# Kernel tuning notes

Measured on AMD Instinct MI355X. Metric: run time of the kernel, lower is better.

The kernel has to match this reference:

```python
import jax, jax.numpy as jnp
import numpy as np

B, SEQ, DIM, HEADS = 2, 2048, 512, 8
HD = DIM // HEADS
RANK, DFF = 128, 1024
TAU_MEM, TAU_ADAPT, SLOPE, EPS = 0.99, 0.95, 25.0, 1e-6
THRESH, ADAPT_STRENGTH = 0.5, 0.1
TREE_LEVELS = int(np.log2(SEQ))  # 11


def rmsnorm(x, w, eps=EPS):
    return x * jax.lax.rsqrt(jnp.mean(x * x, axis=-1, keepdims=True) + eps) * w


def rope_cos_sin(seq, hd):
    inv = 1.0 / (10000.0 ** (jnp.arange(0, hd, 2, dtype=jnp.float32) / hd))
    f = jnp.arange(seq, dtype=jnp.float32)[:, None] * inv[None, :]  # [S, hd/2]
    emb = jnp.concatenate([f, f], axis=-1)  # [S, hd]
    return jnp.cos(emb), jnp.sin(emb)


def apply_rope(x, cos, sin):
    # x: [B, H, S, hd]; rotate-half formulation
    x1, x2 = jnp.split(x, 2, axis=-1)
    return x * cos + jnp.concatenate([-x2, x1], axis=-1) * sin


def setup_inputs() -> dict:
    key = jax.random.key(0)
    ks = jax.random.split(key, 12)
    w = lambda k, shape, fan: (jax.random.normal(k, shape, jnp.float32) / np.sqrt(fan))
    return {
        "x": jax.random.normal(ks[0], (B, SEQ, DIM), jnp.float32),
        "norm_w": jnp.ones((DIM,), jnp.float32),
        "wq": w(ks[1], (DIM, DIM), DIM),
        "wk": w(ks[2], (DIM, DIM), DIM),
        "wv": w(ks[3], (DIM, DIM), DIM),
        "wo": w(ks[4], (DIM, DIM), DIM),
        "lat_w": w(ks[5], (SEQ, SEQ), SEQ),
        "bt": jnp.full((DIM,), THRESH, jnp.float32),
        "as_w": jnp.full((DIM,), ADAPT_STRENGTH, jnp.float32),
        "gate_w": w(ks[6], (DIM, DIM), DIM),
        "tnorm1_w": jnp.ones((DIM,), jnp.float32),
        "tnorm2_w": jnp.ones((DIM,), jnp.float32),
        "ffn_norm_w": jnp.ones((DIM,), jnp.float32),
        "u_w": w(ks[7], (DIM, RANK), DIM),
        "v_w": w(ks[8], (RANK, 2 * DFF), RANK),
        "down_w": w(ks[9], (DFF, DIM), DFF),
    }


def reference(x, norm_w, wq, wk, wv, wo, lat_w, bt, as_w, gate_w,
              tnorm1_w, tnorm2_w, ffn_norm_w, u_w, v_w, down_w):
    Bx, S, D = x.shape
    # --- pre-norm + QKV projections (base_proj) ---
    h = rmsnorm(x, norm_w)
    q = (h @ wq.T).reshape(Bx, S, HEADS, HD).transpose(0, 2, 1, 3)  # [B,H,S,hd]
    k = (h @ wk.T).reshape(Bx, S, HEADS, HD).transpose(0, 2, 1, 3)
    v = (h @ wv.T).reshape(Bx, S, HEADS, HD).transpose(0, 2, 1, 3)
    # --- RoPE ---
    cos, sin = rope_cos_sin(S, HD)
    q = apply_rope(q, cos, sin)
    k = apply_rope(k, cos, sin)
    # --- causal self-attention ---
    scores = jnp.einsum("bhqd,bhkd->bhqk", q, k) / np.sqrt(HD)
    causal = jnp.tril(jnp.ones((S, S), bool))
    scores = jnp.where(causal, scores, jnp.float32(-1e9))
    attn = jnp.einsum("bhqk,bhkd->bhqd", jax.nn.softmax(scores, axis=-1), v)
    attn = attn.transpose(0, 2, 1, 3).reshape(Bx, S, D) @ wo.T
    # --- causal lateral mixing across sequence ---
    mixed = jnp.einsum("ts,bsd->btd", jnp.tril(lat_w), attn)
    # --- ALIF spiking recurrence over the sequence (soft surrogate spike) ---
    def alif_step(carry, i_t):
        vmem, ad = carry
        vmem = TAU_MEM * vmem + i_t
        th = bt + as_w * ad
        spike = jax.nn.sigmoid(SLOPE * (vmem - th))
        vmem = vmem - spike * th          # soft reset
        ad = TAU_ADAPT * ad + spike        # threshold adaptation
        return (vmem, ad), spike
    init = (jnp.zeros((Bx, D), x.dtype), jnp.zeros((Bx, D), x.dtype))
    _, spikes = jax.lax.scan(alif_step, init, mixed.transpose(1, 0, 2))
    spikes = spikes.transpose(1, 0, 2)  # [B,S,D]
    # --- fused addadd residual ---
    h2 = x + mixed + spikes
    # --- binary-tree cell recursion to a root summary ---
    s = h2
    for _ in range(TREE_LEVELS):
        raw = s[:, 0::2, :] + s[:, 1::2, :]         # pairwise sums (raw_sums)
        res = 0.5 * raw                              # residual / prev_s surrogate
        n = rmsnorm(raw, tnorm1_w)
        g = jax.nn.sigmoid(n @ gate_w.T)
        s = rmsnorm(g * n + (1.0 - g) * res, tnorm2_w)
    h3 = h2 + s[:, 0:1, :]  # broadcast root back over the sequence
    # --- low-rank SwiGLU FFN ---
    hn = rmsnorm(h3, ffn_norm_w)
    up = (hn @ u_w) @ v_w                 # [B,S,2*DFF]
    a, b = jnp.split(up, 2, axis=-1)
    ffn = (jax.nn.silu(a) * b) @ down_w   # [B,S,D]
    return h3 + ffn
```

## Files before the change

kernel.cpp:

```cpp
#include <hip/hip_runtime.h>
#include <math.h>

#define BB 2
#define SS 2048
#define DD 512
#define HH 8
#define HDD 64
#define RANKK 128
#define DFFF 1024

typedef short bf16x8 __attribute__((ext_vector_type(8)));
typedef float f32x4 __attribute__((ext_vector_type(4)));

__device__ __forceinline__ short f2b(float f) {
  union { float f; unsigned u; } v; v.f = f;
  unsigned r = v.u + 0x7FFF + ((v.u >> 16) & 1);
  return (short)(r >> 16);
}
__device__ __forceinline__ float b2f(short s) {
  union { unsigned u; float f; } v; v.u = ((unsigned)(unsigned short)s) << 16;
  return v.f;
}

__device__ __forceinline__ void gll16(const void* g, void* l) {
  __builtin_amdgcn_global_load_lds(
      (const __attribute__((address_space(1))) unsigned int*)g,
      (__attribute__((address_space(3))) unsigned int*)l, 16, 0, 0);
}
__device__ __forceinline__ void gll4(const void* g, void* l) {
  __builtin_amdgcn_global_load_lds(
      (const __attribute__((address_space(1))) unsigned int*)g,
      (__attribute__((address_space(3))) unsigned int*)l, 4, 0, 0);
}

__device__ __forceinline__ float wsum(float v) {
#pragma unroll
  for (int off = 32; off > 0; off >>= 1) v += __shfl_xor(v, off, 64);
  return v;
}

__global__ void splitw(const float* __restrict__ in, short* __restrict__ hi,
                       short* __restrict__ lo, int n) {
  int i = (blockIdx.x * 256 + threadIdx.x) * 4;
  if (i >= n) return;
  float4 v = *(const float4*)(in + i);
  short4 h4, l4;
  h4.x = f2b(v.x); l4.x = f2b(v.x - b2f(h4.x));
  h4.y = f2b(v.y); l4.y = f2b(v.y - b2f(h4.y));
  h4.z = f2b(v.z); l4.z = f2b(v.z - b2f(h4.z));
  h4.w = f2b(v.w); l4.w = f2b(v.w - b2f(h4.w));
  *(short4*)(hi + i) = h4;
  *(short4*)(lo + i) = l4;
}

__global__ void cvtb(const float* __restrict__ in, short* __restrict__ out, int n) {
  int i = (blockIdx.x * 256 + threadIdx.x) * 4;
  if (i >= n) return;
  float4 v = *(const float4*)(in + i);
  short4 o; o.x = f2b(v.x); o.y = f2b(v.y); o.z = f2b(v.z); o.w = f2b(v.w);
  *(short4*)(out + i) = o;
}

__global__ void sum2(const float* __restrict__ a, const float* __restrict__ bq,
                     float* __restrict__ o) {
  int i = (blockIdx.x * 256 + threadIdx.x) * 4;
  float4 va = *(const float4*)(a + i);
  float4 vb = *(const float4*)(bq + i);
  float4 vo = {va.x + vb.x, va.y + vb.y, va.z + vb.z, va.w + vb.w};
  *(float4*)(o + i) = vo;
}

__global__ void transp_cvt(const float* __restrict__ in, short* __restrict__ out,
                           int R, int C) {
  __shared__ float t[32][33];
  int c0 = blockIdx.x * 32, r0 = blockIdx.y * 32;
#pragma unroll
  for (int i = 0; i < 4; i++) {
    int idx = threadIdx.x + i * 256;
    int r = idx >> 5, c = idx & 31;
    t[r][c] = in[(size_t)(r0 + r) * C + c0 + c];
  }
  __syncthreads();
#pragma unroll
  for (int i = 0; i < 4; i++) {
    int idx = threadIdx.x + i * 256;
    int cc = idx >> 5, rr = idx & 31;
    out[(size_t)(c0 + cc) * R + r0 + rr] = f2b(t[rr][cc]);
  }
}

__global__ void rmsnorm_hl(const float* __restrict__ x, const float* __restrict__ w,
                           short* __restrict__ oh, short* __restrict__ ol, int rows) {
  int wid = blockIdx.x * 4 + (threadIdx.x >> 6);
  int lane = threadIdx.x & 63;
  if (wid >= rows) return;
  const float* xp = x + (size_t)wid * DD + lane * 8;
  float4 a = *(const float4*)xp;
  float4 b = *(const float4*)(xp + 4);
  float ss = a.x*a.x + a.y*a.y + a.z*a.z + a.w*a.w
           + b.x*b.x + b.y*b.y + b.z*b.z + b.w*b.w;
  ss = wsum(ss);
  float r = rsqrtf(ss * (1.0f / DD) + 1e-6f);
  const float* wp = w + lane * 8;
  float4 wa = *(const float4*)wp, wb = *(const float4*)(wp + 4);
  float o8[8] = {a.x*r*wa.x, a.y*r*wa.y, a.z*r*wa.z, a.w*r*wa.w,
                 b.x*r*wb.x, b.y*r*wb.y, b.z*r*wb.z, b.w*r*wb.w};
  short hv[8], lv[8];
#pragma unroll
  for (int i = 0; i < 8; i++) { hv[i] = f2b(o8[i]); lv[i] = f2b(o8[i] - b2f(hv[i])); }
  short* op = oh + (size_t)wid * DD + lane * 8;
  short* lp = ol + (size_t)wid * DD + lane * 8;
  *(short4*)op = make_short4(hv[0], hv[1], hv[2], hv[3]);
  *(short4*)(op + 4) = make_short4(hv[4], hv[5], hv[6], hv[7]);
  *(short4*)lp = make_short4(lv[0], lv[1], lv[2], lv[3]);
  *(short4*)(lp + 4) = make_short4(lv[4], lv[5], lv[6], lv[7]);
}

template <bool SPL, int OM, bool ROPE>
__global__ __launch_bounds__(256) void ggemm(const short* __restrict__ Ah_g,
                                             const short* __restrict__ Al_g,
                                             const short* __restrict__ Bh_g,
                                             const short* __restrict__ Bl_g,
                                             const float* __restrict__ ADD,
                                             void* __restrict__ C, void* __restrict__ C2,
                                             int M, int N, int K) {
  __shared__ short Ahs[128 * 32];
  __shared__ short Bhs[128 * 32];
  __shared__ short Als[SPL ? 128 * 32 : 8];
  __shared__ short Bls[SPL ? 128 * 32 : 8];
  const int tid = threadIdx.x, l = tid & 63, w = tid >> 6;
  const int wr = (w >> 1) * 64, wc = (w & 1) * 64;
  const int bm = blockIdx.y * 128, bn = blockIdx.x * 128;
  f32x4 acc[4][4] = {};
  for (int k0 = 0; k0 < K; k0 += 32) {
#pragma unroll
    for (int p = 0; p < 2; p++) {
      int row = p * 64 + (tid >> 2), g = tid & 3;
      int swz = (g ^ ((row >> 1) & 3)) * 8;
      gll16(Ah_g + (size_t)(bm + row) * K + k0 + swz, Ahs + p * 2048 + tid * 8);
      gll16(Bh_g + (size_t)(bn + row) * K + k0 + swz, Bhs + p * 2048 + tid * 8);
      if (SPL) {
        gll16(Al_g + (size_t)(bm + row) * K + k0 + swz, Als + p * 2048 + tid * 8);
        gll16(Bl_g + (size_t)(bn + row) * K + k0 + swz, Bls + p * 2048 + tid * 8);
      }
    }
    __syncthreads();
    bf16x8 ah[4], bh[4], al[4], bl[4];
#pragma unroll
    for (int m = 0; m < 4; m++) {
      int r = wr + m * 16 + (l & 15);
      int go = (((l >> 4) ^ ((r >> 1) & 3)) << 3);
      ah[m] = *(const bf16x8*)(Ahs + r * 32 + go);
      if (SPL) al[m] = *(const bf16x8*)(Als + r * 32 + go);
    }
#pragma unroll
    for (int n = 0; n < 4; n++) {
      int r = wc + n * 16 + (l & 15);
      int go = (((l >> 4) ^ ((r >> 1) & 3)) << 3);
      bh[n] = *(const bf16x8*)(Bhs + r * 32 + go);
      if (SPL) bl[n] = *(const bf16x8*)(Bls + r * 32 + go);
    }
#pragma unroll
    for (int m = 0; m < 4; m++)
#pragma unroll
      for (int n = 0; n < 4; n++) {
        acc[m][n] = __builtin_amdgcn_mfma_f32_16x16x32_bf16(ah[m], bh[n], acc[m][n], 0, 0, 0);
        if (SPL) {
          acc[m][n] = __builtin_amdgcn_mfma_f32_16x16x32_bf16(ah[m], bl[n], acc[m][n], 0, 0, 0);
          acc[m][n] = __builtin_amdgcn_mfma_f32_16x16x32_bf16(al[m], bh[n], acc[m][n], 0, 0, 0);
        }
      }
    __syncthreads();
  }
  const int ll = l & 15, lg4 = (l >> 4) * 4;
  if (ROPE) {
#pragma unroll
    for (int m = 0; m < 4; m++)
#pragma unroll
      for (int n = 0; n < 2; n++) {
        int i_ = n * 16 + ll;
        float inv = exp2f(-(float)i_ * (13.287712379549449f / 32.0f));
#pragma unroll
        for (int j = 0; j < 4; j++) {
          int gm = bm + wr + m * 16 + lg4 + j;
          int s = gm & (SS - 1);
          float ang = (float)s * inv;
          float sn, cs;
          sincosf(ang, &sn, &cs);
          float v1 = acc[m][n][j], v2 = acc[m][n + 2][j];
          acc[m][n][j]     = v1 * cs - v2 * sn;
          acc[m][n + 2][j] = v2 * cs + v1 * sn;
        }
      }
  }
#pragma unroll
  for (int m = 0; m < 4; m++)
#pragma unroll
    for (int n = 0; n < 4; n++) {
      int gn = bn + wc + n * 16 + ll;
#pragma unroll
      for (int j = 0; j < 4; j++) {
        int gm = bm + wr + m * 16 + lg4 + j;
        if (gm >= M || gn >= N) continue;
        float v = acc[m][n][j];
        if (OM == 0) {
          ((float*)C)[(size_t)gm * N + gn] = v;
        } else if (OM == 1) {
          ((short*)C)[(size_t)gm * N + gn] = f2b(v);
        } else if (OM == 6) {
          size_t off = (size_t)gm * N + gn;
          ((float*)C)[off] = v + ADD[off];
        } else {
          short hi = f2b(v);
          short lo = f2b(v - b2f(hi));
          int b = gm >> 11, s = gm & (SS - 1);
          int hh2 = gn >> 6, d = gn & 63;
          size_t off;
          if (OM == 2)      off = (((size_t)(b * HH + hh2)) * SS + s) * 64 + d;
          else if (OM == 3) off = (((size_t)(b * HH + hh2)) * 64 + d) * SS + s;
          else              off = ((size_t)(b * DD) + gn) * SS + s;
          ((short*)C)[off] = hi;
          ((short*)C2)[off] = lo;
        }
      }
    }
}

__global__ __launch_bounds__(256) void qkv_g(const short* __restrict__ Ah_g,
                                             const short* __restrict__ Al_g,
                                             const short* __restrict__ wh0, const short* __restrict__ wl0,
                                             const short* __restrict__ wh1, const short* __restrict__ wl1,
                                             const short* __restrict__ wh2, const short* __restrict__ wl2,
                                             short* __restrict__ c0h, short* __restrict__ c0l,
                                             short* __restrict__ c1h, short* __restrict__ c1l,
                                             short* __restrict__ c2h, short* __restrict__ c2l) {
  const int z = blockIdx.z;
  const short* Bh_g = (z == 0) ? wh0 : (z == 1) ? wh1 : wh2;
  const short* Bl_g = (z == 0) ? wl0 : (z == 1) ? wl1 : wl2;
  short* Ch = (z == 0) ? c0h : (z == 1) ? c1h : c2h;
  short* Cl = (z == 0) ? c0l : (z == 1) ? c1l : c2l;
  const int K = DD;
  __shared__ short Ahs[128 * 32];
  __shared__ short Bhs[128 * 32];
  __shared__ short Als[128 * 32];
  __shared__ short Bls[128 * 32];
  const int tid = threadIdx.x, l = tid & 63, w = tid >> 6;
  const int wr = (w >> 1) * 64, wc = (w & 1) * 64;
  const int bm = blockIdx.y * 128, bn = blockIdx.x * 128;
  f32x4 acc[4][4] = {};
  for (int k0 = 0; k0 < K; k0 += 32) {
#pragma unroll
    for (int p = 0; p < 2; p++) {
      int row = p * 64 + (tid >> 2), g = tid & 3;
      int swz = (g ^ ((row >> 1) & 3)) * 8;
      gll16(Ah_g + (size_t)(bm + row) * K + k0 + swz, Ahs + p * 2048 + tid * 8);
      gll16(Bh_g + (size_t)(bn + row) * K + k0 + swz, Bhs + p * 2048 + tid * 8);
      gll16(Al_g + (size_t)(bm + row) * K + k0 + swz, Als + p * 2048 + tid * 8);
      gll16(Bl_g + (size_t)(bn + row) * K + k0 + swz, Bls + p * 2048 + tid * 8);
    }
    __syncthreads();
    bf16x8 ah[4], bh[4], al[4], bl[4];
#pragma unroll
    for (int m = 0; m < 4; m++) {
      int r = wr + m * 16 + (l & 15);
      int go = (((l >> 4) ^ ((r >> 1) & 3)) << 3);
      ah[m] = *(const bf16x8*)(Ahs + r * 32 + go);
      al[m] = *(const bf16x8*)(Als + r * 32 + go);
    }
#pragma unroll
    for (int n = 0; n < 4; n++) {
      int r = wc + n * 16 + (l & 15);
      int go = (((l >> 4) ^ ((r >> 1) & 3)) << 3);
      bh[n] = *(const bf16x8*)(Bhs + r * 32 + go);
      bl[n] = *(const bf16x8*)(Bls + r * 32 + go);
    }
#pragma unroll
    for (int m = 0; m < 4; m++)
#pragma unroll
      for (int n = 0; n < 4; n++) {
        acc[m][n] = __builtin_amdgcn_mfma_f32_16x16x32_bf16(ah[m], bh[n], acc[m][n], 0, 0, 0);
        acc[m][n] = __builtin_amdgcn_mfma_f32_16x16x32_bf16(ah[m], bl[n], acc[m][n], 0, 0, 0);
        acc[m][n] = __builtin_amdgcn_mfma_f32_16x16x32_bf16(al[m], bh[n], acc[m][n], 0, 0, 0);
      }
    __syncthreads();
  }
  const int ll = l & 15, lg4 = (l >> 4) * 4;
  if (z < 2) {
#pragma unroll
    for (int m = 0; m < 4; m++)
#pragma unroll
      for (int n = 0; n < 2; n++) {
        int i_ = n * 16 + ll;
        float inv = exp2f(-(float)i_ * (13.287712379549449f / 32.0f));
#pragma unroll
        for (int j = 0; j < 4; j++) {
          int gm = bm + wr + m * 16 + lg4 + j;
          int s = gm & (SS - 1);
          float ang = (float)s * inv;
          float sn, cs;
          sincosf(ang, &sn, &cs);
          float v1 = acc[m][n][j], v2 = acc[m][n + 2][j];
          acc[m][n][j]     = v1 * cs - v2 * sn;
          acc[m][n + 2][j] = v2 * cs + v1 * sn;
        }
      }
  }
#pragma unroll
  for (int m = 0; m < 4; m++)
#pragma unroll
    for (int n = 0; n < 4; n++) {
      int gn = bn + wc + n * 16 + ll;
#pragma unroll
      for (int j = 0; j < 4; j++) {
        int gm = bm + wr + m * 16 + lg4 + j;
        float v = acc[m][n][j];
        short hi = f2b(v);
        short lo = f2b(v - b2f(hi));
        int b = gm >> 11, s = gm & (SS - 1);
        int hh2 = gn >> 6, d = gn & 63;
        size_t off = (z < 2) ? ((((size_t)(b * HH + hh2)) * SS + s) * 64 + d)
                             : ((((size_t)(b * HH + hh2)) * 64 + d) * SS + s);
        Ch[off] = hi;
        Cl[off] = lo;
      }
    }
}

__global__ __launch_bounds__(256) void lat_g(const float* __restrict__ lat,
                                             const short* __restrict__ bTh,
                                             const short* __restrict__ bTl,
                                             float* __restrict__ P0,
                                             float* __restrict__ P1) {
  const int zb = blockIdx.z >> 1;
  const int half = blockIdx.z & 1;
  bTh += (size_t)zb * DD * SS;
  bTl += (size_t)zb * DD * SS;
  float* Cc = (half == 0 ? P0 : P1) + (size_t)zb * DD * SS;
  __shared__ short Ah[128 * 32];
  __shared__ short Al[128 * 32];
  __shared__ short Bh[128 * 32];
  __shared__ short Bl[128 * 32];
  const int tid = threadIdx.x, l = tid & 63, w = tid >> 6;
  const int wr = (w >> 1) * 64, wc = (w & 1) * 64;
  const int bm = blockIdx.y * 128, bn = blockIdx.x * 128;
  const int T = blockIdx.y + 1;
  const int h0 = (T + 1) >> 1;
  const int kbeg = (half == 0) ? 0 : h0 * 128;
  const int kend = (half == 0) ? h0 * 128 : T * 128;
  f32x4 acc[4][4] = {};
  const int ll = l & 15, lg4 = (l >> 4) * 4;
  for (int k0 = kbeg; k0 < kend; k0 += 32) {
#pragma unroll
    for (int p = 0; p < 2; p++) {
      int row = p * 64 + (tid >> 2), g = tid & 3;
      int swz = (g ^ ((row >> 1) & 3)) * 8;
      gll16(bTh + (size_t)(bn + row) * SS + k0 + swz, Bh + p * 2048 + tid * 8);
      gll16(bTl + (size_t)(bn + row) * SS + k0 + swz, Bl + p * 2048 + tid * 8);
    }
#pragma unroll
    for (int i = 0; i < 4; i++) {
      int lin = i * 256 + tid;
      int row = lin >> 3, f4 = lin & 7;
      int gr = bm + row;
      float4 v = *(const float4*)(lat + (size_t)gr * SS + k0 + f4 * 4);
      int kc = k0 + f4 * 4;
      if (kc + 0 > gr) v.x = 0.0f;
      if (kc + 1 > gr) v.y = 0.0f;
      if (kc + 2 > gr) v.z = 0.0f;
      if (kc + 3 > gr) v.w = 0.0f;
      int off = row * 32 + (((f4 >> 1) ^ ((row >> 1) & 3)) << 3) + (f4 & 1) * 4;
      short4 hh, lo;
      hh.x = f2b(v.x); lo.x = f2b(v.x - b2f(hh.x));
      hh.y = f2b(v.y); lo.y = f2b(v.y - b2f(hh.y));
      hh.z = f2b(v.z); lo.z = f2b(v.z - b2f(hh.z));
      hh.w = f2b(v.w); lo.w = f2b(v.w - b2f(hh.w));
      *(short4*)(Ah + off) = hh;
      *(short4*)(Al + off) = lo;
    }
    __syncthreads();
    bf16x8 ah[4], bh[4], al[4], bl[4];
#pragma unroll
    for (int m = 0; m < 4; m++) {
      int r = wr + m * 16 + (l & 15);
      int go = (((l >> 4) ^ ((r >> 1) & 3)) << 3);
      ah[m] = *(const bf16x8*)(Ah + r * 32 + go);
      al[m] = *(const bf16x8*)(Al + r * 32 + go);
    }
#pragma unroll
    for (int n = 0; n < 4; n++) {
      int r = wc + n * 16 + (l & 15);
      int go = (((l >> 4) ^ ((r >> 1) & 3)) << 3);
      bh[n] = *(const bf16x8*)(Bh + r * 32 + go);
      bl[n] = *(const bf16x8*)(Bl + r * 32 + go);
    }
#pragma unroll
    for (int m = 0; m < 4; m++)
#pragma unroll
      for (int n = 0; n < 4; n++) {
        acc[m][n] = __builtin_amdgcn_mfma_f32_16x16x32_bf16(ah[m], bh[n], acc[m][n], 0, 0, 0);
        acc[m][n] = __builtin_amdgcn_mfma_f32_16x16x32_bf16(ah[m], bl[n], acc[m][n], 0, 0, 0);
        acc[m][n] = __builtin_amdgcn_mfma_f32_16x16x32_bf16(al[m], bh[n], acc[m][n], 0, 0, 0);
      }
    __syncthreads();
  }
#pragma unroll
  for (int m = 0; m < 4; m++)
#pragma unroll
    for (int n = 0; n < 4; n++) {
      int gn = bn + wc + n * 16 + ll;
#pragma unroll
      for (int j = 0; j < 4; j++) {
        int gm = bm + wr + m * 16 + lg4 + j;
        Cc[(size_t)gn * SS + gm] = acc[m][n][j];
      }
    }
}

__global__ __launch_bounds__(256) void attn_g(const short* __restrict__ qh,
                                              const short* __restrict__ ql,
                                              const short* __restrict__ kh,
                                              const short* __restrict__ kl,
                                              const short* __restrict__ vh,
                                              const short* __restrict__ vl,
                                              short* __restrict__ aho,
                                              short* __restrict__ alo) {
  const int h = blockIdx.y, b = blockIdx.z;
  const int qt = (b == 0) ? (int)blockIdx.x : 31 - (int)blockIdx.x;
  const int q0 = qt * 64;
  const int tid = threadIdx.x, w = tid >> 6, l = tid & 63;
  const int lg = l >> 4, ll = l & 15;
  __shared__ short Kh[64 * 64], Kl[64 * 64];
  __shared__ short Vh[64 * 64], Vl[64 * 64];
  __shared__ short Ph[64 * 64], Pl[64 * 64];
  const size_t bh = (size_t)(b * HH + h);

  const int qr = q0 + w * 16 + ll;
  const short* qbh = qh + (bh * SS + qr) * 64;
  const short* qbl = ql + (bh * SS + qr) * 64;
  bf16x8 qfh[2], qfl[2];
#pragma unroll
  for (int ks = 0; ks < 2; ks++) {
    qfh[ks] = *(const bf16x8*)(qbh + (ks * 4 + lg) * 8);
    qfl[ks] = *(const bf16x8*)(qbl + (ks * 4 + lg) * 8);
  }

  f32x4 o[4] = {};
  float mrow[4] = {-1e30f, -1e30f, -1e30f, -1e30f};
  float lsum[4] = {};
  const int qrow0 = q0 + w * 16 + lg * 4;
  const int ntiles = qt + 1;

  for (int kt = 0; kt < ntiles; kt++) {
#pragma unroll
    for (int p = 0; p < 2; p++) {
      int row = p * 32 + (tid >> 3), g = tid & 7;
      int sw = ((g ^ (row & 7)) << 3);
      size_t krow = (bh * SS + kt * 64 + row) * 64;
      size_t vrow = (bh * 64 + row) * SS + kt * 64;
      gll16(kh + krow + sw, Kh + p * 2048 + tid * 8);
      gll16(kl + krow + sw, Kl + p * 2048 + tid * 8);
      gll16(vh + vrow + sw, Vh + p * 2048 + tid * 8);
      gll16(vl + vrow + sw, Vl + p * 2048 + tid * 8);
    }
    __syncthreads();

    f32x4 sv[4] = {};
#pragma unroll
    for (int nf = 0; nf < 4; nf++) {
      int r = nf * 16 + ll;
#pragma unroll
      for (int ks = 0; ks < 2; ks++) {
        int g = (ks * 4 + lg) ^ (r & 7);
        bf16x8 khf = *(const bf16x8*)(Kh + r * 64 + g * 8);
        bf16x8 klf = *(const bf16x8*)(Kl + r * 64 + g * 8);
        sv[nf] = __builtin_amdgcn_mfma_f32_16x16x32_bf16(qfh[ks], khf, sv[nf], 0, 0, 0);
        sv[nf] = __builtin_amdgcn_mfma_f32_16x16x32_bf16(qfh[ks], klf, sv[nf], 0, 0, 0);
        sv[nf] = __builtin_amdgcn_mfma_f32_16x16x32_bf16(qfl[ks], khf, sv[nf], 0, 0, 0);
      }
    }
#pragma unroll
    for (int nf = 0; nf < 4; nf++) {
      int kpos = kt * 64 + nf * 16 + ll;
#pragma unroll
      for (int j = 0; j < 4; j++) {
        float v = sv[nf][j] * 0.125f;
        sv[nf][j] = (kpos > qrow0 + j) ? -1e30f : v;
      }
    }
    float cf[4];
#pragma unroll
    for (int j = 0; j < 4; j++) {
      float r = fmaxf(fmaxf(sv[0][j], sv[1][j]), fmaxf(sv[2][j], sv[3][j]));
      r = fmaxf(r, __shfl_xor(r, 1)); r = fmaxf(r, __shfl_xor(r, 2));
      r = fmaxf(r, __shfl_xor(r, 4)); r = fmaxf(r, __shfl_xor(r, 8));
      float mn = fmaxf(mrow[j], r);
      cf[j] = __expf(mrow[j] - mn);
      mrow[j] = mn;
    }
    float ps[4] = {};
#pragma unroll
    for (int nf = 0; nf < 4; nf++)
#pragma unroll
      for (int j = 0; j < 4; j++) {
        float p = __expf(sv[nf][j] - mrow[j]);
        sv[nf][j] = p;
        ps[j] += p;
      }
#pragma unroll
    for (int j = 0; j < 4; j++) {
      float r = ps[j];
      r += __shfl_xor(r, 1); r += __shfl_xor(r, 2);
      r += __shfl_xor(r, 4); r += __shfl_xor(r, 8);
      lsum[j] = lsum[j] * cf[j] + r;
    }
#pragma unroll
    for (int nf = 0; nf < 4; nf++)
#pragma unroll
      for (int j = 0; j < 4; j++) o[nf][j] *= cf[j];
#pragma unroll
    for (int nf = 0; nf < 4; nf++)
#pragma unroll
      for (int j = 0; j < 4; j++) {
        int rowP = w * 16 + lg * 4 + j;
        int col = nf * 16 + ll;
        int off = rowP * 64 + (((col >> 3) ^ (rowP & 7)) << 3) + (col & 7);
        float p = sv[nf][j];
        short hi = f2b(p);
        Ph[off] = hi;
        Pl[off] = f2b(p - b2f(hi));
      }
    __syncthreads();
    bf16x8 pfh[2], pfl[2];
    {
      int rowA = w * 16 + ll;
#pragma unroll
      for (int ks = 0; ks < 2; ks++) {
        int g = (ks * 4 + lg) ^ (rowA & 7);
        pfh[ks] = *(const bf16x8*)(Ph + rowA * 64 + g * 8);
        pfl[ks] = *(const bf16x8*)(Pl + rowA * 64 + g * 8);
      }
    }
#pragma unroll
    for (int nf = 0; nf < 4; nf++) {
      int r = nf * 16 + ll;
#pragma unroll
      for (int ks = 0; ks < 2; ks++) {
        int g = (ks * 4 + lg) ^ (r & 7);
        bf16x8 vhf = *(const bf16x8*)(Vh + r * 64 + g * 8);
        bf16x8 vlf = *(const bf16x8*)(Vl + r * 64 + g * 8);
        o[nf] = __builtin_amdgcn_mfma_f32_16x16x32_bf16(pfh[ks], vhf, o[nf], 0, 0, 0);
        o[nf] = __builtin_amdgcn_mfma_f32_16x16x32_bf16(pfh[ks], vlf, o[nf], 0, 0, 0);
        o[nf] = __builtin_amdgcn_mfma_f32_16x16x32_bf16(pfl[ks], vhf, o[nf], 0, 0, 0);
      }
    }
    __syncthreads();
  }
  float inv[4];
#pragma unroll
  for (int j = 0; j < 4; j++) inv[j] = 1.0f / lsum[j];
#pragma unroll
  for (int nf = 0; nf < 4; nf++)
#pragma unroll
    for (int j = 0; j < 4; j++) {
      float v = o[nf][j] * inv[j];
      short hi = f2b(v);
      size_t off = ((size_t)(b * SS + qrow0 + j)) * DD + h * HDD + nf * 16 + ll;
      aho[off] = hi;
      alo[off] = f2b(v - b2f(hi));
    }
}

#define ACH 32
__global__ __launch_bounds__(64, 1) void tsa_alif5(const float* __restrict__ mixedT,
                                                   const float* __restrict__ bt,
                                                   const float* __restrict__ asw,
                                                   float* __restrict__ spikesT) {
  __shared__ float lds[2][ACH * 64];
  const int t = threadIdx.x;
  const int tid = blockIdx.x * 64 + t;
  const int b = tid >> 9, d = tid & 511;
  const float btd = bt[d], asd = asw[d];
  const float C = 36.06737602222409f;
  const float bt36 = btd * C, as36 = asd * C;
  const float bt99 = 0.99f * btd, as99 = 0.99f * asd;
  const size_t base = ((size_t)(b * DD + d)) * SS;
  const float* mp = mixedT + base;
  float* sp = spikesT + base;
#pragma unroll
  for (int j = 0; j < ACH; j++) gll4(mp + j, &lds[0][j * 64]);
  float vR = 0.0f, ad = 0.0f;
  for (int c = 0; c < SS / ACH; c++) {
    const int cur = c & 1;
    __syncthreads();
    if (c + 1 < SS / ACH) {
      const float* q = mp + (c + 1) * ACH;
#pragma unroll
      for (int j = 0; j < ACH; j++) gll4(q + j, &lds[cur ^ 1][j * 64]);
    }
    float m[ACH];
#pragma unroll
    for (int j = 0; j < ACH; j++) m[j] = lds[cur][j * 64 + t];
    vR += m[0];
    float sO[ACH];
#pragma unroll
    for (int j = 0; j < ACH; j++) {
      float thC = fmaf(ad, as36, bt36);
      float th99 = fmaf(ad, as99, bt99);
      float arg = fmaf(vR, -C, thC);
      float e = exp2f(arg);
      float s = __builtin_amdgcn_rcpf(1.0f + e);
      sO[j] = s;
      float pre = (j + 1 < ACH) ? fmaf(0.99f, vR, m[j + 1]) : (0.99f * vR);
      vR = fmaf(-th99, s, pre);
      ad = fmaf(0.95f, ad, s);
      if ((j & 3) == 3) {
        float4 o4 = {sO[j - 3], sO[j - 2], sO[j - 1], sO[j]};
        *(float4*)(sp + c * ACH + (j - 3)) = o4;
      }
    }
  }
}

__global__ __launch_bounds__(256) void fuse_h2(const float* __restrict__ x,
                                               const float* __restrict__ mixedT,
                                               const float* __restrict__ spikesT,
                                               float* __restrict__ h2) {
  const int s0 = blockIdx.x * 64, d0 = blockIdx.y * 64, b = blockIdx.z;
  __shared__ float t[64][65];
#pragma unroll
  for (int k = 0; k < 4; k++) {
    int dl = threadIdx.x >> 2;
    int sl = (threadIdx.x & 3) * 16 + k * 4;
    size_t off = ((size_t)(b * DD + d0 + dl)) * SS + s0 + sl;
    float4 mv = *(const float4*)(mixedT + off);
    float4 sv = *(const float4*)(spikesT + off);
    t[dl][sl + 0] = mv.x + sv.x;
    t[dl][sl + 1] = mv.y + sv.y;
    t[dl][sl + 2] = mv.z + sv.z;
    t[dl][sl + 3] = mv.w + sv.w;
  }
  __syncthreads();
#pragma unroll
  for (int k = 0; k < 4; k++) {
    int sl = threadIdx.x >> 2;
    int dl = (threadIdx.x & 3) * 16 + k * 4;
    size_t off = ((size_t)(b * SS + s0 + sl)) * DD + d0 + dl;
    float4 xv = *(const float4*)(x + off);
    float4 o;
    o.x = xv.x + t[dl + 0][sl];
    o.y = xv.y + t[dl + 1][sl];
    o.z = xv.z + t[dl + 2][sl];
    o.w = xv.w + t[dl + 3][sl];
    *(float4*)(h2 + off) = o;
  }
}

__global__ void tree_reduce_b(const float* __restrict__ sin_, const float* __restrict__ tn1,
                              short* __restrict__ nb, int Sn) {
  int wid = blockIdx.x * 4 + (threadIdx.x >> 6);
  int lane = threadIdx.x & 63;
  int rows = BB * Sn;
  if (wid >= rows) return;
  int b = wid / Sn, j = wid - b * Sn;
  const float* r0 = sin_ + ((size_t)(b * 2 * Sn + 2 * j)) * DD + lane * 8;
  const float* r1 = r0 + DD;
  float4 a0 = *(const float4*)r0, a1 = *(const float4*)(r0 + 4);
  float4 b0 = *(const float4*)r1, b1 = *(const float4*)(r1 + 4);
  float ra[8] = {a0.x + b0.x, a0.y + b0.y, a0.z + b0.z, a0.w + b0.w,
                 a1.x + b1.x, a1.y + b1.y, a1.z + b1.z, a1.w + b1.w};
  float ss = 0.0f;
#pragma unroll
  for (int i = 0; i < 8; i++) ss += ra[i] * ra[i];
  ss = wsum(ss);
  float rms = rsqrtf(ss * (1.0f / DD) + 1e-6f);
  const float* wp = tn1 + lane * 8;
  float4 wa = *(const float4*)wp, wb = *(const float4*)(wp + 4);
  float wv8[8] = {wa.x, wa.y, wa.z, wa.w, wb.x, wb.y, wb.z, wb.w};
  short* np = nb + (size_t)wid * DD + lane * 8;
  short4 n0, n1;
  n0.x = f2b(ra[0]*rms*wv8[0]); n0.y = f2b(ra[1]*rms*wv8[1]);
  n0.z = f2b(ra[2]*rms*wv8[2]); n0.w = f2b(ra[3]*rms*wv8[3]);
  n1.x = f2b(ra[4]*rms*wv8[4]); n1.y = f2b(ra[5]*rms*wv8[5]);
  n1.z = f2b(ra[6]*rms*wv8[6]); n1.w = f2b(ra[7]*rms*wv8[7]);
  *(short4*)np = n0;
  *(short4*)(np + 4) = n1;
}

__global__ void tree_combine_b(const float* __restrict__ g, const short* __restrict__ nb,
                               const float* __restrict__ sin_, const float* __restrict__ tn2,
                               float* __restrict__ sout, int Sn) {
  int wid = blockIdx.x * 4 + (threadIdx.x >> 6);
  int lane = threadIdx.x & 63;
  int rows = BB * Sn;
  if (wid >= rows) return;
  int b = wid / Sn, j = wid - b * Sn;
  const float* r0 = sin_ + ((size_t)(b * 2 * Sn + 2 * j)) * DD + lane * 8;
  const float* r1 = r0 + DD;
  float4 a0 = *(const float4*)r0, a1 = *(const float4*)(r0 + 4);
  float4 b0 = *(const float4*)r1, b1 = *(const float4*)(r1 + 4);
  float res[8] = {0.5f*(a0.x + b0.x), 0.5f*(a0.y + b0.y), 0.5f*(a0.z + b0.z), 0.5f*(a0.w + b0.w),
                  0.5f*(a1.x + b1.x), 0.5f*(a1.y + b1.y), 0.5f*(a1.z + b1.z), 0.5f*(a1.w + b1.w)};
  size_t base = (size_t)wid * DD + lane * 8;
  float t[8];
  float ss = 0.0f;
#pragma unroll
  for (int i = 0; i < 8; i++) {
    float gg = 1.0f / (1.0f + expf(-g[base + i]));
    float tv = gg * b2f(nb[base + i]) + (1.0f - gg) * res[i];
    t[i] = tv;
    ss += tv * tv;
  }
  ss = wsum(ss);
  float rms = rsqrtf(ss * (1.0f / DD) + 1e-6f);
#pragma unroll
  for (int i = 0; i < 8; i++) sout[base + i] = t[i] * rms * tn2[lane * 8 + i];
}

__global__ void h3hn_b(const float* __restrict__ h2, const float* __restrict__ root,
                       const float* __restrict__ fw, float* __restrict__ h3,
                       short* __restrict__ hn) {
  int wid = blockIdx.x * 4 + (threadIdx.x >> 6);
  int lane = threadIdx.x & 63;
  int b = wid >> 11;
  size_t base = (size_t)wid * DD + lane * 8;
  const float* rp = root + (size_t)b * DD + lane * 8;
  float t[8];
  float ss = 0.0f;
#pragma unroll
  for (int i = 0; i < 8; i++) {
    float tv = h2[base + i] + rp[i];
    t[i] = tv;
    ss += tv * tv;
    h3[base + i] = tv;
  }
  ss = wsum(ss);
  float rms = rsqrtf(ss * (1.0f / DD) + 1e-6f);
#pragma unroll
  for (int i = 0; i < 8; i++) hn[base + i] = f2b(t[i] * rms * fw[lane * 8 + i]);
}

__global__ __launch_bounds__(256) void upgate_g(const short* __restrict__ A,
                                                const short* __restrict__ Bv,
                                                short* __restrict__ ffa) {
  __shared__ short Ahs[128 * 32];
  __shared__ short B1s[128 * 32];
  __shared__ short B2s[128 * 32];
  const int tid = threadIdx.x, l = tid & 63, w = tid >> 6;
  const int wr = (w >> 1) * 64, wc = (w & 1) * 64;
  const int bm = blockIdx.y * 128, bn = blockIdx.x * 128;
  f32x4 acc1[4][4] = {}, acc2[4][4] = {};
  for (int k0 = 0; k0 < RANKK; k0 += 32) {
#pragma unroll
    for (int p = 0; p < 2; p++) {
      int row = p * 64 + (tid >> 2), g = tid & 3;
      int swz = (g ^ ((row >> 1) & 3)) * 8;
      gll16(A + (size_t)(bm + row) * RANKK + k0 + swz, Ahs + p * 2048 + tid * 8);
      gll16(Bv + (size_t)(bn + row) * RANKK + k0 + swz, B1s + p * 2048 + tid * 8);
      gll16(Bv + (size_t)(DFFF + bn + row) * RANKK + k0 + swz, B2s + p * 2048 + tid * 8);
    }
    __syncthreads();
    bf16x8 ah[4], b1[4], b2[4];
#pragma unroll
    for (int m = 0; m < 4; m++) {
      int r = wr + m * 16 + (l & 15);
      int go = (((l >> 4) ^ ((r >> 1) & 3)) << 3);
      ah[m] = *(const bf16x8*)(Ahs + r * 32 + go);
    }
#pragma unroll
    for (int n = 0; n < 4; n++) {
      int r = wc + n * 16 + (l & 15);
      int go = (((l >> 4) ^ ((r >> 1) & 3)) << 3);
      b1[n] = *(const bf16x8*)(B1s + r * 32 + go);
      b2[n] = *(const bf16x8*)(B2s + r * 32 + go);
    }
#pragma unroll
    for (int m = 0; m < 4; m++)
#pragma unroll
      for (int n = 0; n < 4; n++) {
        acc1[m][n] = __builtin_amdgcn_mfma_f32_16x16x32_bf16(ah[m], b1[n], acc1[m][n], 0, 0, 0);
        acc2[m][n] = __builtin_amdgcn_mfma_f32_16x16x32_bf16(ah[m], b2[n], acc2[m][n], 0, 0, 0);
      }
    __syncthreads();
  }
#pragma unroll
  for (int m = 0; m < 4; m++)
#pragma unroll
    for (int n = 0; n < 4; n++) {
      int gn = bn + wc + n * 16 + (l & 15);
#pragma unroll
      for (int j = 0; j < 4; j++) {
        int gm = bm + wr + m * 16 + (l >> 4) * 4 + j;
        float a = acc1[m][n][j];
        float s = a / (1.0f + __expf(-a));
        ffa[(size_t)gm * DFFF + gn] = f2b(s * acc2[m][n][j]);
      }
    }
}

extern "C" void kernel_launch(void* const* d_in, const int* in_sizes, int n_in,
                              void* d_out, int out_size, void* d_ws, size_t ws_size,
                              hipStream_t stream) {
  const float* x   = (const float*)d_in[0];
  const float* nw  = (const float*)d_in[1];
  const float* wq  = (const float*)d_in[2];
  const float* wk  = (const float*)d_in[3];
  const float* wv  = (const float*)d_in[4];
  const float* wo  = (const float*)d_in[5];
  const float* lat = (const float*)d_in[6];
  const float* btp = (const float*)d_in[7];
  const float* asw = (const float*)d_in[8];
  const float* gw  = (const float*)d_in[9];
  const float* tn1 = (const float*)d_in[10];
  const float* tn2 = (const float*)d_in[11];
  const float* fnw = (const float*)d_in[12];
  const float* uw  = (const float*)d_in[13];
  const float* vw  = (const float*)d_in[14];
  const float* dw  = (const float*)d_in[15];
  float* out = (float*)d_out;
  char* W = (char*)d_ws;
  const size_t MB = 1u << 20;

  short* h_hi = (short*)(W);
  short* h_lo = (short*)(W + 4 * MB);
  short* attn_hi = h_hi;
  short* attn_lo = h_lo;
  short* nb = (short*)(W);
  float* gb = (float*)(W + 2 * MB);
  short* q_hi = (short*)(W + 8 * MB);
  short* q_lo = (short*)(W + 12 * MB);
  short* apT_hi = q_hi;
  short* apT_lo = q_lo;
  float* spikesT = (float*)(W + 8 * MB);
  float* s0 = (float*)(W + 8 * MB);
  float* s1 = (float*)(W + 12 * MB);
  short* k_hi = (short*)(W + 16 * MB);
  short* k_lo = (short*)(W + 20 * MB);
  float* latP1 = (float*)(W + 16 * MB);
  short* hn = (short*)(W + 16 * MB);
  short* t1 = (short*)(W + 20 * MB);
  short* v_hi = (short*)(W + 24 * MB);
  short* v_lo = (short*)(W + 28 * MB);
  float* h2 = (float*)(W + 24 * MB);
  short* ffa = (short*)(W + 24 * MB);
  float* latP0 = (float*)(W + 32 * MB);
  short* gwb = (short*)(W + 32 * MB);
  short* uwT = gwb + 262144;
  short* vwT = uwT + 65536;
  short* dwT = vwT + 262144;

  short* wqh = (short*)out;
  short* wql = wqh + 262144;
  short* wkh = wql + 262144;
  short* wkl = wkh + 262144;
  short* wvh = wkl + 262144;
  short* wvl = wvh + 262144;
  short* woh = wvl + 262144;
  short* wol = woh + 262144;

  const int rows = BB * SS;

  splitw<<<256, 256, 0, stream>>>(wq, wqh, wql, DD * DD);
  splitw<<<256, 256, 0, stream>>>(wk, wkh, wkl, DD * DD);
  splitw<<<256, 256, 0, stream>>>(wv, wvh, wvl, DD * DD);
  splitw<<<256, 256, 0, stream>>>(wo, woh, wol, DD * DD);

  rmsnorm_hl<<<rows / 4, 256, 0, stream>>>(x, nw, h_hi, h_lo, rows);

  qkv_g<<<dim3(4, 32, 3), 256, 0, stream>>>(h_hi, h_lo,
                                            wqh, wql, wkh, wkl, wvh, wvl,
                                            q_hi, q_lo, k_hi, k_lo, v_hi, v_lo);

  attn_g<<<dim3(32, HH, BB), 256, 0, stream>>>(q_hi, q_lo, k_hi, k_lo, v_hi, v_lo,
                                               attn_hi, attn_lo);

  ggemm<true, 4, false><<<dim3(4, 32), 256, 0, stream>>>(
      attn_hi, attn_lo, woh, wol, nullptr, apT_hi, apT_lo, rows, DD, DD);

  lat_g<<<dim3(4, 16, 4), 256, 0, stream>>>(lat, apT_hi, apT_lo, latP0, latP1);

  sum2<<<(BB * DD * SS / 4) / 256, 256, 0, stream>>>(latP0, latP1, latP0);

  tsa_alif5<<<16, 64, 0, stream>>>(latP0, btp, asw, spikesT);
  fuse_h2<<<dim3(32, 8, 2), 256, 0, stream>>>(x, latP0, spikesT, h2);

  cvtb<<<256, 256, 0, stream>>>(gw, gwb, DD * DD);
  transp_cvt<<<dim3(4, 16), 256, 0, stream>>>(uw, uwT, DD, RANKK);
  transp_cvt<<<dim3(64, 4), 256, 0, stream>>>(vw, vwT, RANKK, 2 * DFFF);
  transp_cvt<<<dim3(16, 32), 256, 0, stream>>>(dw, dwT, DFFF, DD);

  const float* sin_ = h2;
  for (int lvl = 0; lvl < 11; lvl++) {
    int Sn = 1024 >> lvl;
    int r2 = BB * Sn;
    float* sout = (lvl & 1) ? s1 : s0;
    tree_reduce_b<<<(r2 + 3) / 4, 256, 0, stream>>>(sin_, tn1, nb, Sn);
    ggemm<false, 0, false><<<dim3(4, (r2 + 127) / 128), 256, 0, stream>>>(
        nb, nullptr, gwb, nullptr, nullptr, gb, nullptr, r2, DD, DD);
    tree_combine_b<<<(r2 + 3) / 4, 256, 0, stream>>>(gb, nb, sin_, tn2, sout, Sn);
    sin_ = sout;
  }

  h3hn_b<<<rows / 4, 256, 0, stream>>>(h2, sin_, fnw, out, hn);

  ggemm<false, 1, false><<<dim3(1, 32), 256, 0, stream>>>(
      hn, nullptr, uwT, nullptr, nullptr, t1, nullptr, rows, RANKK, DD);
  upgate_g<<<dim3(8, 32), 256, 0, stream>>>(t1, vwT, ffa);
  ggemm<false, 6, false><<<dim3(4, 32), 256, 0, stream>>>(
      ffa, nullptr, dwT, nullptr, out, out, nullptr, rows, DD, DFFF);
}
```

Before: 679.9 us.

## Use chunked swizzled layout for lateral-mix output so ALIF scan loads coalesce

```diff
diff --git a/kernel.cpp b/kernel.cpp
--- a/kernel.cpp
+++ b/kernel.cpp
@@ -26,11 +26,6 @@
   __builtin_amdgcn_global_load_lds(
       (const __attribute__((address_space(1))) unsigned int*)g,
       (__attribute__((address_space(3))) unsigned int*)l, 16, 0, 0);
-}
-__device__ __forceinline__ void gll4(const void* g, void* l) {
-  __builtin_amdgcn_global_load_lds(
-      (const __attribute__((address_space(1))) unsigned int*)g,
-      (__attribute__((address_space(3))) unsigned int*)l, 4, 0, 0);
 }
 
 __device__ __forceinline__ float wsum(float v) {
@@ -411,7 +406,8 @@
 #pragma unroll
       for (int j = 0; j < 4; j++) {
         int gm = bm + wr + m * 16 + lg4 + j;
-        Cc[(size_t)gn * SS + gm] = acc[m][n][j];
+        size_t off = ((size_t)((gm >> 5) * 512 + gn)) * 32 + ((gm + gn) & 31);
+        Cc[off] = acc[m][n][j];
       }
     }
 }
@@ -571,35 +567,37 @@
 }
 
 #define ACH 32
-__global__ __launch_bounds__(64, 1) void tsa_alif5(const float* __restrict__ mixedT,
-                                                   const float* __restrict__ bt,
-                                                   const float* __restrict__ asw,
-                                                   float* __restrict__ spikesT) {
+__global__ __launch_bounds__(64) void tsa_alif6(const float* __restrict__ mixedS,
+                                                const float* __restrict__ bt,
+                                                const float* __restrict__ asw,
+                                                float* __restrict__ spikesS) {
   __shared__ float lds[2][ACH * 64];
   const int t = threadIdx.x;
   const int tid = blockIdx.x * 64 + t;
   const int b = tid >> 9, d = tid & 511;
+  const int d0 = d & ~63;
   const float btd = bt[d], asd = asw[d];
   const float C = 36.06737602222409f;
   const float bt36 = btd * C, as36 = asd * C;
   const float bt99 = 0.99f * btd, as99 = 0.99f * asd;
-  const size_t base = ((size_t)(b * DD + d)) * SS;
-  const float* mp = mixedT + base;
-  float* sp = spikesT + base;
-#pragma unroll
-  for (int j = 0; j < ACH; j++) gll4(mp + j, &lds[0][j * 64]);
+  const size_t bbase = (size_t)b * DD * SS;
+  {
+    const float* g0 = mixedS + bbase + (size_t)d0 * 32;
+#pragma unroll
+    for (int i = 0; i < 8; i++) gll16(g0 + i * 256 + t * 4, &lds[0][i * 256 + t * 4]);
+  }
   float vR = 0.0f, ad = 0.0f;
   for (int c = 0; c < SS / ACH; c++) {
     const int cur = c & 1;
     __syncthreads();
     if (c + 1 < SS / ACH) {
-      const float* q = mp + (c + 1) * ACH;
-#pragma unroll
-      for (int j = 0; j < ACH; j++) gll4(q + j, &lds[cur ^ 1][j * 64]);
+      const float* gq = mixedS + bbase + ((size_t)((c + 1) * 512 + d0)) * 32;
+#pragma unroll
+      for (int i = 0; i < 8; i++) gll16(gq + i * 256 + t * 4, &lds[cur ^ 1][i * 256 + t * 4]);
     }
     float m[ACH];
 #pragma unroll
-    for (int j = 0; j < ACH; j++) m[j] = lds[cur][j * 64 + t];
+    for (int j = 0; j < ACH; j++) m[j] = lds[cur][t * 32 + ((j + t) & 31)];
     vR += m[0];
     float sO[ACH];
 #pragma unroll
@@ -613,44 +611,47 @@
       float pre = (j + 1 < ACH) ? fmaf(0.99f, vR, m[j + 1]) : (0.99f * vR);
       vR = fmaf(-th99, s, pre);
       ad = fmaf(0.95f, ad, s);
-      if ((j & 3) == 3) {
-        float4 o4 = {sO[j - 3], sO[j - 2], sO[j - 1], sO[j]};
-        *(float4*)(sp + c * ACH + (j - 3)) = o4;
-      }
+    }
+#pragma unroll
+    for (int j = 0; j < ACH; j++) lds[cur][t * 32 + ((j + t) & 31)] = sO[j];
+    __syncthreads();
+    float* so = spikesS + bbase + ((size_t)(c * 512 + d0)) * 32;
+#pragma unroll
+    for (int i = 0; i < 8; i++) {
+      float4 v4 = *(const float4*)&lds[cur][i * 256 + t * 4];
+      *(float4*)(so + i * 256 + t * 4) = v4;
     }
   }
 }
 
 __global__ __launch_bounds__(256) void fuse_h2(const float* __restrict__ x,
-                                               const float* __restrict__ mixedT,
-                                               const float* __restrict__ spikesT,
+                                               const float* __restrict__ mixedS,
+                                               const float* __restrict__ spikesS,
                                                float* __restrict__ h2) {
   const int s0 = blockIdx.x * 64, d0 = blockIdx.y * 64, b = blockIdx.z;
   __shared__ float t[64][65];
-#pragma unroll
-  for (int k = 0; k < 4; k++) {
-    int dl = threadIdx.x >> 2;
-    int sl = (threadIdx.x & 3) * 16 + k * 4;
-    size_t off = ((size_t)(b * DD + d0 + dl)) * SS + s0 + sl;
-    float4 mv = *(const float4*)(mixedT + off);
-    float4 sv = *(const float4*)(spikesT + off);
-    t[dl][sl + 0] = mv.x + sv.x;
-    t[dl][sl + 1] = mv.y + sv.y;
-    t[dl][sl + 2] = mv.z + sv.z;
-    t[dl][sl + 3] = mv.w + sv.w;
+  const int dl = threadIdx.x >> 2;
+  const int grp = threadIdx.x & 3;
+  const size_t bbase = (size_t)b * DD * SS;
+#pragma unroll
+  for (int i = 0; i < 16; i++) {
+    int sl = grp * 16 + i;
+    int sg = s0 + sl;
+    size_t off = bbase + ((size_t)((sg >> 5) * 512 + d0 + dl)) * 32 + ((sg + dl) & 31);
+    t[dl][sl] = mixedS[off] + spikesS[off];
   }
   __syncthreads();
 #pragma unroll
   for (int k = 0; k < 4; k++) {
     int sl = threadIdx.x >> 2;
-    int dl = (threadIdx.x & 3) * 16 + k * 4;
-    size_t off = ((size_t)(b * SS + s0 + sl)) * DD + d0 + dl;
+    int dl2 = (threadIdx.x & 3) * 16 + k * 4;
+    size_t off = ((size_t)(b * SS + s0 + sl)) * DD + d0 + dl2;
     float4 xv = *(const float4*)(x + off);
     float4 o;
-    o.x = xv.x + t[dl + 0][sl];
-    o.y = xv.y + t[dl + 1][sl];
-    o.z = xv.z + t[dl + 2][sl];
-    o.w = xv.w + t[dl + 3][sl];
+    o.x = xv.x + t[dl2 + 0][sl];
+    o.y = xv.y + t[dl2 + 1][sl];
+    o.z = xv.z + t[dl2 + 2][sl];
+    o.w = xv.w + t[dl2 + 3][sl];
     *(float4*)(h2 + off) = o;
   }
 }
@@ -830,7 +831,7 @@
   short* q_lo = (short*)(W + 12 * MB);
   short* apT_hi = q_hi;
   short* apT_lo = q_lo;
-  float* spikesT = (float*)(W + 8 * MB);
+  float* spikesS = (float*)(W + 8 * MB);
   float* s0 = (float*)(W + 8 * MB);
   float* s1 = (float*)(W + 12 * MB);
   short* k_hi = (short*)(W + 16 * MB);
@@ -880,8 +881,8 @@
 
   sum2<<<(BB * DD * SS / 4) / 256, 256, 0, stream>>>(latP0, latP1, latP0);
 
-  tsa_alif5<<<16, 64, 0, stream>>>(latP0, btp, asw, spikesT);
-  fuse_h2<<<dim3(32, 8, 2), 256, 0, stream>>>(x, latP0, spikesT, h2);
+  tsa_alif6<<<16, 64, 0, stream>>>(latP0, btp, asw, spikesS);
+  fuse_h2<<<dim3(32, 8, 2), 256, 0, stream>>>(x, latP0, spikesS, h2);
 
   cvtb<<<256, 256, 0, stream>>>(gw, gwb, DD * DD);
   transp_cvt<<<dim3(4, 16), 256, 0, stream>>>(uw, uwT, DD, RANKK);
```

New measurement: 686.1 us. About the same (+0.9%).
